# Optimization experiments

Measured on AMD Instinct MI355X. Metric: run time of the kernel, lower is better.

Reference implementation:

```python
import jax, jax.numpy as jnp
import numpy as np

# FFT-based (Makhoul) inverse DCT-II along the last axis.
#   y_n = X_0/2 + sum_{k=1}^{N-1} X_k * cos(pi*k*(2n+1)/(2N))
# expk is the complex twiddle exp(1j*pi*k/(2N)), k = 0..N-1.

def _idct_last(X, expk):
    N = X.shape[-1]
    # X_{N-k} with the k=0 slot set to 0
    Xr = jnp.concatenate([jnp.zeros_like(X[..., :1]), jnp.flip(X[..., 1:], axis=-1)], axis=-1)
    V = 0.5 * (X - 1j * Xr) * expk              # half-spectrum with twiddles
    v = jnp.fft.ifft(V, axis=-1).real * N        # undo jnp.fft's 1/N
    h = N // 2                                   # N assumed even (grid dims are)
    # de-interleave: y_{2m} = v_m, y_{2m+1} = v_{N-1-m}
    y = jnp.stack([v[..., :h], jnp.flip(v, axis=-1)[..., :h]], axis=-1)
    return y.reshape(X.shape)


def _idxst_last(X, expk):
    # y_n = sum_{k=1}^{N-1} X_k * sin(pi*k*(2n+1)/(2N))
    #     = (-1)^n * IDCT(X')_n  with X'_k = X_{N-k}, X'_0 = 0
    N = X.shape[-1]
    Xf = jnp.concatenate([jnp.zeros_like(X[..., :1]), jnp.flip(X[..., 1:], axis=-1)], axis=-1)
    sign = jnp.where(jnp.arange(N) % 2 == 0, 1.0, -1.0).astype(X.dtype)
    return sign * _idct_last(Xf, expk)


def setup_inputs() -> dict:
    key = jax.random.key(0)
    B, M, N = 2, 4096, 4096
    x = jax.random.normal(key, (B, M, N), dtype=jnp.float32)

    def make_expk(K):
        k = np.arange(K, dtype=np.float64)
        ang = np.pi * k / (2.0 * K)
        return jnp.asarray(np.stack([np.cos(ang), np.sin(ang)], axis=-1), dtype=jnp.float32)

    return {"x": x, "expkM": make_expk(M), "expkN": make_expk(N)}


def reference(x, expkM, expkN):
    ekM = expkM[:, 0] + 1j * expkM[:, 1]   # exp(1j*pi*k/(2M))
    ekN = expkN[:, 0] + 1j * expkN[:, 1]   # exp(1j*pi*k/(2N))
    # IDCT along the M (row) dimension: move it to last axis
    y = _idct_last(jnp.swapaxes(x, -1, -2), ekM)
    y = jnp.swapaxes(y, -1, -2)
    # IDXST along the N (column) dimension
    return _idxst_last(y, ekN)
```

## Files before the change

### kernel.cpp

```cpp
#include <hip/hip_runtime.h>

#define PI_F 3.14159265358979323846f

__device__ __forceinline__ float2 cmulf(float2 a, float c, float s) {
    return make_float2(a.x * c - a.y * s, a.x * s + a.y * c);
}

template<bool IDXST>
__global__ __launch_bounds__(256)
void row_fft_kernel(const float* in, float* out, const float2* expk)
{
    __shared__ float smem[8192];
    float*  xs = smem;
    float2* za = (float2*)(smem + 4096);
    float2* zb = (float2*)smem;

    const int t = threadIdx.x;
    const size_t row = blockIdx.x;
    const float* src = in  + row * 4096;
    float*       dst = out + row * 4096;

    {
        const float4* s4 = (const float4*)src;
        float4* x4 = (float4*)xs;
        #pragma unroll
        for (int i = 0; i < 4; i++) x4[t + 256 * i] = s4[t + 256 * i];
    }
    __syncthreads();

    #pragma unroll
    for (int i = 0; i < 8; i++) {
        int k = t + 256 * i;
        float Xa, Xra, Xb, Xrb;
        if (IDXST) {
            Xa  = (k == 0) ? 0.0f : xs[4096 - k];
            Xra = (k == 0) ? 0.0f : xs[k];
            Xb  = xs[2048 - k];
            Xrb = xs[k + 2048];
        } else {
            Xa  = xs[k];
            Xra = (k == 0) ? 0.0f : xs[4096 - k];
            Xb  = xs[k + 2048];
            Xrb = xs[2048 - k];
        }
        float2 ea = expk[k];
        float2 eb = expk[k + 2048];
        float Var = 0.5f * (Xa * ea.x + Xra * ea.y);
        float Vai = 0.5f * (Xa * ea.y - Xra * ea.x);
        float Vbr = 0.5f * (Xb * eb.x + Xrb * eb.y);
        float Vbi = 0.5f * (Xb * eb.y - Xrb * eb.x);
        float Ar = Var + Vbr, Ai = Vai + Vbi;
        float Dr = Var - Vbr, Di = Vai - Vbi;
        float cw, sw;
        __sincosf(PI_F * (float)k * (1.0f / 2048.0f), &sw, &cw);
        float Br = Dr * cw - Di * sw;
        float Bi = Dr * sw + Di * cw;
        za[k] = make_float2(Ar - Bi, Ai + Br);
    }
    __syncthreads();

    float2* sb = za;
    float2* db = zb;
    int Ns = 1;
    #pragma unroll
    for (int s = 0; s < 5; s++) {
        int ls = 2 * s;
        #pragma unroll
        for (int ii = 0; ii < 2; ii++) {
            int j = t + 256 * ii;
            float2 v0 = sb[j];
            float2 v1 = sb[j + 512];
            float2 v2 = sb[j + 1024];
            float2 v3 = sb[j + 1536];
            int jm = j & (Ns - 1);
            float ang = (0.5f * PI_F) * (float)jm / (float)Ns;
            float s1, c1;
            __sincosf(ang, &s1, &c1);
            float c2 = c1 * c1 - s1 * s1, s2 = 2.0f * c1 * s1;
            float c3 = c1 * c2 - s1 * s2, s3 = c1 * s2 + s1 * c2;
            v1 = cmulf(v1, c1, s1);
            v2 = cmulf(v2, c2, s2);
            v3 = cmulf(v3, c3, s3);
            float2 a0 = make_float2(v0.x + v2.x, v0.y + v2.y);
            float2 a1 = make_float2(v0.x - v2.x, v0.y - v2.y);
            float2 a2 = make_float2(v1.x + v3.x, v1.y + v3.y);
            float2 a3 = make_float2(v1.x - v3.x, v1.y - v3.y);
            int idxD = ((j >> ls) << (ls + 2)) | jm;
            db[idxD]          = make_float2(a0.x + a2.x, a0.y + a2.y);
            db[idxD + Ns]     = make_float2(a1.x - a3.y, a1.y + a3.x);
            db[idxD + 2 * Ns] = make_float2(a0.x - a2.x, a0.y - a2.y);
            db[idxD + 3 * Ns] = make_float2(a1.x + a3.y, a1.y - a3.x);
        }
        __syncthreads();
        float2* tmp = sb; sb = db; db = tmp;
        Ns <<= 2;
    }
    #pragma unroll
    for (int ii = 0; ii < 4; ii++) {
        int j = t + 256 * ii;
        float2 v0 = sb[j];
        float2 v1 = sb[j + 1024];
        float s1, c1;
        __sincosf(PI_F * (float)j * (1.0f / 1024.0f), &s1, &c1);
        v1 = cmulf(v1, c1, s1);
        db[j]        = make_float2(v0.x + v1.x, v0.y + v1.y);
        db[j + 1024] = make_float2(v0.x - v1.x, v0.y - v1.y);
    }
    __syncthreads();
    const float2* zf = db;

    float4* d4 = (float4*)dst;
    #pragma unroll
    for (int i = 0; i < 4; i++) {
        int p = t + 256 * i;
        float2 zp = zf[p];
        float2 zq = zf[2047 - p];
        float4 o;
        if (IDXST) {
            o.x = zp.x; o.y = -zq.y; o.z = zp.y; o.w = -zq.x;
        } else {
            o.x = zp.x; o.y =  zq.y; o.z = zp.y; o.w =  zq.x;
        }
        d4[p] = o;
    }
}

__global__ __launch_bounds__(256)
void transpose_inplace(float* d, int n)
{
    __shared__ float ta[64][65];
    __shared__ float tb[64][65];
    int ti = blockIdx.x, tj = blockIdx.y, b = blockIdx.z;
    if (tj < ti) return;
    float* base = d + (size_t)b * n * n;
    int x  = threadIdx.x;
    int y0 = threadIdx.y;
    size_t offA = (size_t)(ti * 64) * n + tj * 64;
    size_t offB = (size_t)(tj * 64) * n + ti * 64;

    #pragma unroll
    for (int r = y0; r < 64; r += 4) ta[r][x] = base[offA + (size_t)r * n + x];
    if (ti != tj) {
        #pragma unroll
        for (int r = y0; r < 64; r += 4) tb[r][x] = base[offB + (size_t)r * n + x];
    }
    __syncthreads();
    if (ti != tj) {
        #pragma unroll
        for (int r = y0; r < 64; r += 4) {
            base[offA + (size_t)r * n + x] = tb[x][r];
            base[offB + (size_t)r * n + x] = ta[x][r];
        }
    } else {
        #pragma unroll
        for (int r = y0; r < 64; r += 4) base[offA + (size_t)r * n + x] = ta[x][r];
    }
}

extern "C" void kernel_launch(void* const* d_in, const int* in_sizes, int n_in,
                              void* d_out, int out_size, void* d_ws, size_t ws_size,
                              hipStream_t stream)
{
    const float*  x     = (const float*)d_in[0];
    const float2* expkM = (const float2*)d_in[1];
    const float2* expkN = (const float2*)d_in[2];
    float* out = (float*)d_out;

    const int B = in_sizes[0] / (4096 * 4096);
    const int rows = B * 4096;

    row_fft_kernel<true><<<rows, 256, 0, stream>>>(x, out, expkN);
    transpose_inplace<<<dim3(64, 64, B), dim3(64, 4), 0, stream>>>(out, 4096);
    row_fft_kernel<false><<<rows, 256, 0, stream>>>(out, out, expkM);
    transpose_inplace<<<dim3(64, 64, B), dim3(64, 4), 0, stream>>>(out, 4096);
}
```

Before: 378.4 us.

## Restructure row FFT with register first stage, twiddle tables, swizzled LDS, vectorized transpose

```diff
diff --git a/kernel.cpp b/kernel.cpp
--- a/kernel.cpp
+++ b/kernel.cpp
@@ -1,47 +1,40 @@
 #include <hip/hip_runtime.h>
-
-#define PI_F 3.14159265358979323846f
 
 __device__ __forceinline__ float2 cmulf(float2 a, float c, float s) {
     return make_float2(a.x * c - a.y * s, a.x * s + a.y * c);
 }
 
+#define SW(e) ((e) ^ ((e) >> 4))
+
 template<bool IDXST>
 __global__ __launch_bounds__(256)
-void row_fft_kernel(const float* in, float* out, const float2* expk)
+void row_fft_kernel(const float* in, float* out, const float2* __restrict__ expk)
 {
-    __shared__ float smem[8192];
-    float*  xs = smem;
-    float2* za = (float2*)(smem + 4096);
-    float2* zb = (float2*)smem;
+    __shared__ float2 bufA[2048];
+    __shared__ float2 bufB[2048];
 
     const int t = threadIdx.x;
     const size_t row = blockIdx.x;
     const float* src = in  + row * 4096;
     float*       dst = out + row * 4096;
 
-    {
-        const float4* s4 = (const float4*)src;
-        float4* x4 = (float4*)xs;
-        #pragma unroll
-        for (int i = 0; i < 4; i++) x4[t + 256 * i] = s4[t + 256 * i];
-    }
-    __syncthreads();
-
+    float2 z[8];
     #pragma unroll
     for (int i = 0; i < 8; i++) {
         int k = t + 256 * i;
         float Xa, Xra, Xb, Xrb;
         if (IDXST) {
-            Xa  = (k == 0) ? 0.0f : xs[4096 - k];
-            Xra = (k == 0) ? 0.0f : xs[k];
-            Xb  = xs[2048 - k];
-            Xrb = xs[k + 2048];
+            Xa  = src[(4096 - k) & 4095];
+            Xra = src[k];
+            Xb  = src[2048 - k];
+            Xrb = src[2048 + k];
+            if (k == 0) { Xa = 0.0f; Xra = 0.0f; }
         } else {
-            Xa  = xs[k];
-            Xra = (k == 0) ? 0.0f : xs[4096 - k];
-            Xb  = xs[k + 2048];
-            Xrb = xs[2048 - k];
+            Xa  = src[k];
+            Xra = src[(4096 - k) & 4095];
+            Xb  = src[2048 + k];
+            Xrb = src[2048 - k];
+            if (k == 0) Xra = 0.0f;
         }
         float2 ea = expk[k];
         float2 eb = expk[k + 2048];
@@ -51,77 +44,95 @@
         float Vbi = 0.5f * (Xb * eb.y - Xrb * eb.x);
         float Ar = Var + Vbr, Ai = Vai + Vbi;
         float Dr = Var - Vbr, Di = Vai - Vbi;
-        float cw, sw;
-        __sincosf(PI_F * (float)k * (1.0f / 2048.0f), &sw, &cw);
+        int k4 = 4 * k;
+        float2 et = expk[k4 & 4095];
+        bool hi = (k4 >= 4096);
+        float cw = hi ? -et.y : et.x;
+        float sw = hi ?  et.x : et.y;
         float Br = Dr * cw - Di * sw;
         float Bi = Dr * sw + Di * cw;
-        za[k] = make_float2(Ar - Bi, Ai + Br);
+        z[i] = make_float2(Ar - Bi, Ai + Br);
+    }
+
+    #pragma unroll
+    for (int ii = 0; ii < 2; ii++) {
+        float2 v0 = z[ii], v1 = z[ii + 2], v2 = z[ii + 4], v3 = z[ii + 6];
+        float a0r = v0.x + v2.x, a0i = v0.y + v2.y;
+        float a1r = v0.x - v2.x, a1i = v0.y - v2.y;
+        float a2r = v1.x + v3.x, a2i = v1.y + v3.y;
+        float a3r = v1.x - v3.x, a3i = v1.y - v3.y;
+        int idxD = (t + 256 * ii) << 2;
+        bufA[SW(idxD)]     = make_float2(a0r + a2r, a0i + a2i);
+        bufA[SW(idxD + 1)] = make_float2(a1r - a3i, a1i + a3r);
+        bufA[SW(idxD + 2)] = make_float2(a0r - a2r, a0i - a2i);
+        bufA[SW(idxD + 3)] = make_float2(a1r + a3i, a1i - a3r);
     }
     __syncthreads();
 
-    float2* sb = za;
-    float2* db = zb;
-    int Ns = 1;
-    #pragma unroll
-    for (int s = 0; s < 5; s++) {
-        int ls = 2 * s;
+    float2* sb = bufA;
+    float2* db = bufB;
+    int Ns = 4;
+    #pragma unroll
+    for (int s = 1; s < 5; s++) {
+        const int ls = 2 * s;
+        const int shift = 12 - 2 * s;
         #pragma unroll
         for (int ii = 0; ii < 2; ii++) {
             int j = t + 256 * ii;
-            float2 v0 = sb[j];
-            float2 v1 = sb[j + 512];
-            float2 v2 = sb[j + 1024];
-            float2 v3 = sb[j + 1536];
+            float2 v0 = sb[SW(j)];
+            float2 v1 = sb[SW(j + 512)];
+            float2 v2 = sb[SW(j + 1024)];
+            float2 v3 = sb[SW(j + 1536)];
             int jm = j & (Ns - 1);
-            float ang = (0.5f * PI_F) * (float)jm / (float)Ns;
-            float s1, c1;
-            __sincosf(ang, &s1, &c1);
+            float2 e1 = expk[jm << shift];
+            float c1 = e1.x, s1 = e1.y;
             float c2 = c1 * c1 - s1 * s1, s2 = 2.0f * c1 * s1;
             float c3 = c1 * c2 - s1 * s2, s3 = c1 * s2 + s1 * c2;
             v1 = cmulf(v1, c1, s1);
             v2 = cmulf(v2, c2, s2);
             v3 = cmulf(v3, c3, s3);
-            float2 a0 = make_float2(v0.x + v2.x, v0.y + v2.y);
-            float2 a1 = make_float2(v0.x - v2.x, v0.y - v2.y);
-            float2 a2 = make_float2(v1.x + v3.x, v1.y + v3.y);
-            float2 a3 = make_float2(v1.x - v3.x, v1.y - v3.y);
+            float a0r = v0.x + v2.x, a0i = v0.y + v2.y;
+            float a1r = v0.x - v2.x, a1i = v0.y - v2.y;
+            float a2r = v1.x + v3.x, a2i = v1.y + v3.y;
+            float a3r = v1.x - v3.x, a3i = v1.y - v3.y;
             int idxD = ((j >> ls) << (ls + 2)) | jm;
-            db[idxD]          = make_float2(a0.x + a2.x, a0.y + a2.y);
-            db[idxD + Ns]     = make_float2(a1.x - a3.y, a1.y + a3.x);
-            db[idxD + 2 * Ns] = make_float2(a0.x - a2.x, a0.y - a2.y);
-            db[idxD + 3 * Ns] = make_float2(a1.x + a3.y, a1.y - a3.x);
+            db[SW(idxD)]          = make_float2(a0r + a2r, a0i + a2i);
+            db[SW(idxD + Ns)]     = make_float2(a1r - a3i, a1i + a3r);
+            db[SW(idxD + 2 * Ns)] = make_float2(a0r - a2r, a0i - a2i);
+            db[SW(idxD + 3 * Ns)] = make_float2(a1r + a3i, a1i - a3r);
         }
         __syncthreads();
         float2* tmp = sb; sb = db; db = tmp;
         Ns <<= 2;
     }
-    #pragma unroll
-    for (int ii = 0; ii < 4; ii++) {
-        int j = t + 256 * ii;
-        float2 v0 = sb[j];
-        float2 v1 = sb[j + 1024];
-        float s1, c1;
-        __sincosf(PI_F * (float)j * (1.0f / 1024.0f), &s1, &c1);
-        v1 = cmulf(v1, c1, s1);
-        db[j]        = make_float2(v0.x + v1.x, v0.y + v1.y);
-        db[j + 1024] = make_float2(v0.x - v1.x, v0.y - v1.y);
-    }
-    __syncthreads();
-    const float2* zf = db;
 
     float4* d4 = (float4*)dst;
     #pragma unroll
-    for (int i = 0; i < 4; i++) {
-        int p = t + 256 * i;
-        float2 zp = zf[p];
-        float2 zq = zf[2047 - p];
-        float4 o;
+    for (int ii = 0; ii < 2; ii++) {
+        int j  = t + 256 * ii;
+        int jB = 1023 - j;
+        float2 a0 = sb[SW(j)];
+        float2 a1 = sb[SW(j + 1024)];
+        float2 b0 = sb[SW(jB)];
+        float2 b1 = sb[SW(jB + 1024)];
+        float2 eA = expk[8 * j];
+        float2 eB = expk[8 * (511 - j)];
+        float2 wa1 = cmulf(a1, eA.x, eA.y);
+        float2 wb1 = cmulf(b1, -eB.y, eB.x);
+        float2 zA0 = make_float2(a0.x + wa1.x, a0.y + wa1.y);
+        float2 zA1 = make_float2(a0.x - wa1.x, a0.y - wa1.y);
+        float2 zB0 = make_float2(b0.x + wb1.x, b0.y + wb1.y);
+        float2 zB1 = make_float2(b0.x - wb1.x, b0.y - wb1.y);
+        float4 oA, oB;
         if (IDXST) {
-            o.x = zp.x; o.y = -zq.y; o.z = zp.y; o.w = -zq.x;
+            oA = make_float4(zA0.x, -zB1.y, zA0.y, -zB1.x);
+            oB = make_float4(zB0.x, -zA1.y, zB0.y, -zA1.x);
         } else {
-            o.x = zp.x; o.y =  zq.y; o.z = zp.y; o.w =  zq.x;
-        }
-        d4[p] = o;
+            oA = make_float4(zA0.x,  zB1.y, zA0.y,  zB1.x);
+            oB = make_float4(zB0.x,  zA1.y, zB0.y,  zA1.x);
+        }
+        d4[j]  = oA;
+        d4[jB] = oB;
     }
 }
 
@@ -133,27 +144,52 @@
     int ti = blockIdx.x, tj = blockIdx.y, b = blockIdx.z;
     if (tj < ti) return;
     float* base = d + (size_t)b * n * n;
-    int x  = threadIdx.x;
-    int y0 = threadIdx.y;
+    const int t  = threadIdx.x;
+    const int c4 = t & 15;
+    const int r0 = t >> 4;
     size_t offA = (size_t)(ti * 64) * n + tj * 64;
     size_t offB = (size_t)(tj * 64) * n + ti * 64;
 
     #pragma unroll
-    for (int r = y0; r < 64; r += 4) ta[r][x] = base[offA + (size_t)r * n + x];
+    for (int q = 0; q < 4; q++) {
+        int r = r0 + 16 * q;
+        float4 va = ((const float4*)(base + offA + (size_t)r * n))[c4];
+        ta[r][4 * c4 + 0] = va.x; ta[r][4 * c4 + 1] = va.y;
+        ta[r][4 * c4 + 2] = va.z; ta[r][4 * c4 + 3] = va.w;
+    }
     if (ti != tj) {
         #pragma unroll
-        for (int r = y0; r < 64; r += 4) tb[r][x] = base[offB + (size_t)r * n + x];
+        for (int q = 0; q < 4; q++) {
+            int r = r0 + 16 * q;
+            float4 vb = ((const float4*)(base + offB + (size_t)r * n))[c4];
+            tb[r][4 * c4 + 0] = vb.x; tb[r][4 * c4 + 1] = vb.y;
+            tb[r][4 * c4 + 2] = vb.z; tb[r][4 * c4 + 3] = vb.w;
+        }
     }
     __syncthreads();
+
     if (ti != tj) {
         #pragma unroll
-        for (int r = y0; r < 64; r += 4) {
-            base[offA + (size_t)r * n + x] = tb[x][r];
-            base[offB + (size_t)r * n + x] = ta[x][r];
+        for (int q = 0; q < 4; q++) {
+            int r = r0 + 16 * q;
+            float4 o;
+            o.x = tb[4 * c4 + 0][r]; o.y = tb[4 * c4 + 1][r];
+            o.z = tb[4 * c4 + 2][r]; o.w = tb[4 * c4 + 3][r];
+            ((float4*)(base + offA + (size_t)r * n))[c4] = o;
+            float4 p;
+            p.x = ta[4 * c4 + 0][r]; p.y = ta[4 * c4 + 1][r];
+            p.z = ta[4 * c4 + 2][r]; p.w = ta[4 * c4 + 3][r];
+            ((float4*)(base + offB + (size_t)r * n))[c4] = p;
         }
     } else {
         #pragma unroll
-        for (int r = y0; r < 64; r += 4) base[offA + (size_t)r * n + x] = ta[x][r];
+        for (int q = 0; q < 4; q++) {
+            int r = r0 + 16 * q;
+            float4 p;
+            p.x = ta[4 * c4 + 0][r]; p.y = ta[4 * c4 + 1][r];
+            p.z = ta[4 * c4 + 2][r]; p.w = ta[4 * c4 + 3][r];
+            ((float4*)(base + offA + (size_t)r * n))[c4] = p;
+        }
     }
 }
 
@@ -170,7 +206,7 @@
     const int rows = B * 4096;
 
     row_fft_kernel<true><<<rows, 256, 0, stream>>>(x, out, expkN);
-    transpose_inplace<<<dim3(64, 64, B), dim3(64, 4), 0, stream>>>(out, 4096);
+    transpose_inplace<<<dim3(64, 64, B), dim3(256), 0, stream>>>(out, 4096);
     row_fft_kernel<false><<<rows, 256, 0, stream>>>(out, out, expkM);
-    transpose_inplace<<<dim3(64, 64, B), dim3(64, 4), 0, stream>>>(out, 4096);
-}
+    transpose_inplace<<<dim3(64, 64, B), dim3(256), 0, stream>>>(out, 4096);
+}
```

Measured after the change: 438.5 us. +15.9%, slower.
